# Optimization experiments

Measured on AMD Instinct MI355X. Metric: run time of the kernel, lower is better.

## Reference

```python
import jax, jax.numpy as jnp
import numpy as np

EPSILON = 1e-6
SEARCH_RADIUS = 11 // 2  # search_window_size=11 -> 121 shifts
PATCH_RADIUS = 5 // 2    # patch_size=5 box sum


def shift_stack(t, r):
    # Matches ShiftStack: outer loop x_shift, inner loop y_shift, roll dims (H,W)=(2,3).
    # t: [B,C,H,W] -> [B,C,H,W,(2r+1)^2]
    return jnp.stack(
        [jnp.roll(t, (dy, dx), axis=(2, 3))
         for dx in range(-r, r + 1) for dy in range(-r, r + 1)],
        axis=-1,
    )


def box_sum(t, r):
    # Circular box-filter sum over a (2r+1)x(2r+1) window; separable form is
    # mathematically identical to the original 25 rolls (rolls commute/add).
    s = sum(jnp.roll(t, d, axis=2) for d in range(-r, r + 1))
    return sum(jnp.roll(s, d, axis=3) for d in range(-r, r + 1))


def setup_inputs() -> dict:
    key = jax.random.key(0)
    k1, k2 = jax.random.split(key)
    rgb = jax.random.uniform(k1, (1, 3, 512, 512), dtype=jnp.float32)
    # realistic noise std in [0.02, 0.12]
    sigma = jax.random.uniform(k2, (1, 1, 1, 1), dtype=jnp.float32) * 0.1 + 0.02
    return {"rgb": rgb, "sigma": sigma}


def reference(rgb, sigma):
    h = sigma * 2.0                                     # [B,1,1,1]
    y = 0.299 * rgb[:, :1] + 0.587 * rgb[:, 1:2] + 0.114 * rgb[:, 2:]  # [B,1,H,W]
    rgb_stack = shift_stack(rgb, SEARCH_RADIUS)         # [B,3,H,W,K]
    y_stack = shift_stack(y, SEARCH_RADIUS)             # [B,1,H,W,K]
    sq_diff = (y[..., None] - y_stack) ** 2             # [B,1,H,W,K]
    distances = jnp.sqrt(box_sum(sq_diff, PATCH_RADIUS))
    weights = jnp.exp(-distances / (jax.nn.relu(h)[..., None] + EPSILON))  # [B,1,H,W,K]
    denoised = (weights * rgb_stack).sum(axis=-1) / weights.sum(axis=-1)   # [B,3,H,W]
    return jnp.clip(denoised, 0.0, 1.0)
```

## Files before the change

### kernel.cpp

```cpp
#include <hip/hip_runtime.h>
#include <math.h>

#define IH 512
#define IW 512
#define NPX (IH*IW)

#define TW 60
#define BH 16
#define NXT 9
#define YROWS 30
#define YCOLS 74
#define YSZ2 (YROWS*YCOLS)
#define RROWS 26
#define RCOLS 74
#define RCH2 (RROWS*RCOLS)

#define TS 32
#define YHALO 7
#define RHALO 5
#define YD (TS + 2*YHALO)
#define RD (TS + 2*RHALO)
#define RSZ (RD*RD)
#define MYSZ (YD*YD)

#define FSQRT(x) __builtin_amdgcn_sqrtf(x)
#if __has_builtin(__builtin_amdgcn_exp2f)
#define FEXP2(x) __builtin_amdgcn_exp2f(x)
#else
#define FEXP2(x) exp2f(x)
#endif

__device__ __forceinline__ float dpp_shl1(float x) {
    return __int_as_float(__builtin_amdgcn_update_dpp(
        0, __float_as_int(x), 0x130, 0xf, 0xf, true));
}

__global__ __launch_bounds__(256)
void nlm_part(const float* __restrict__ rgb,
              const float* __restrict__ sigma,
              float4* __restrict__ ws) {
    __shared__ float  YL[YSZ2];
    __shared__ float4 RGBL4[RCH2];

    const int tid   = threadIdx.x;
    const int lane  = tid & 63;
    const int wavei = tid >> 6;
    const int tx0 = blockIdx.x * TW;
    const int ty0 = blockIdx.y * BH;
    const int slice = blockIdx.z;
    const int nz = gridDim.z;

    const float* Rp = rgb;
    const float* Gp = rgb + NPX;
    const float* Bp = rgb + 2*NPX;

    for (int idx = tid; idx < YSZ2; idx += 256) {
        int a = idx / YCOLS, b = idx - a*YCOLS;
        int gy = (ty0 + a - 7) & (IH-1);
        int gx = (tx0 + b - 7) & (IW-1);
        int g = gy*IW + gx;
        YL[idx] = 0.299f*Rp[g] + 0.587f*Gp[g] + 0.114f*Bp[g];
    }
    for (int idx = tid; idx < RCH2; idx += 256) {
        int a = idx / RCOLS, b = idx - a*RCOLS;
        int gy = (ty0 + a - 5) & (IH-1);
        int gx = (tx0 + b - 5) & (IW-1);
        int g = gy*IW + gx;
        RGBL4[idx] = make_float4(Rp[g], Gp[g], Bp[g], 0.f);
    }
    __syncthreads();

    const float m2 = -1.4426950408889634f /
                     (fmaxf(sigma[0]*2.0f, 0.0f) + 1e-6f);

    const int l  = lane;
    const int r0 = wavei*4;

    float yb8[8];
    #pragma unroll
    for (int i = 0; i < 8; ++i)
        yb8[i] = YL[(r0+5+i)*YCOLS + (l+5)];

    float accR[4]={0,0,0,0}, accG[4]={0,0,0,0},
          accB[4]={0,0,0,0}, den[4]={0,0,0,0};

    int dxlo, dxcnt;
    if (nz == 6) { if (slice < 5) { dxlo = -5 + 2*slice; dxcnt = 2; }
                   else           { dxlo = 5;            dxcnt = 1; } }
    else         { if (slice < 3) { dxlo = -5 + 3*slice; dxcnt = 3; }
                   else           { dxlo = 4;            dxcnt = 2; } }

    for (int u = 0; u < dxcnt; ++u) {
        const int dx = dxlo + u;
        const int ysb   = r0*YCOLS + (l + 5 - dx);
        const int rgb_b = r0*RCOLS + (l + 5 - dx);

        float sub8[8];
        #pragma unroll
        for (int j = 0; j < 8; ++j)
            sub8[j] = YL[ysb + j*YCOLS];

        float4 rgbw[4];
        #pragma unroll
        for (int s = 0; s < 4; ++s)
            rgbw[s] = RGBL4[rgb_b + s*RCOLS];

        #pragma unroll
        for (int k = 0; k <= 10; ++k) {
            if (k > 0) {
                sub8[(k+7)&7] = YL[ysb + (7+k)*YCOLS];
                rgbw[(k+3)&3] = RGBL4[rgb_b + (k+3)*RCOLS];
            }
            float pre[9]; pre[0] = 0.f;
            #pragma unroll
            for (int i = 0; i < 8; ++i) {
                float d = yb8[i] - sub8[(i+k)&7];
                pre[i+1] = fmaf(d, d, pre[i]);
            }
            float V[4];
            #pragma unroll
            for (int rr = 0; rr < 4; ++rr) V[rr] = pre[rr+5] - pre[rr];

            float box[4];
            #pragma unroll
            for (int rr = 0; rr < 4; ++rr) {
                float s1 = dpp_shl1(V[rr]);
                float s2 = dpp_shl1(s1);
                float s3 = dpp_shl1(s2);
                float s4 = dpp_shl1(s3);
                box[rr] = ((V[rr] + s1) + (s2 + s3)) + s4;
            }
            #pragma unroll
            for (int rr = 0; rr < 4; ++rr) {
                float w = FEXP2(FSQRT(fmaxf(box[rr], 0.f)) * m2);
                float4 p = rgbw[(k+rr)&3];
                accR[rr] = fmaf(w, p.x, accR[rr]);
                accG[rr] = fmaf(w, p.y, accG[rr]);
                accB[rr] = fmaf(w, p.z, accB[rr]);
                den[rr] += w;
            }
        }
    }

    if (l < TW && tx0 + l < IW) {
        #pragma unroll
        for (int rr = 0; rr < 4; ++rr) {
            int px = (ty0 + r0 + rr)*IW + tx0 + l;
            ws[(size_t)slice*NPX + px] =
                make_float4(accR[rr], accG[rr], accB[rr], den[rr]);
        }
    }
}

__global__ __launch_bounds__(256)
void nlm_combine(const float4* __restrict__ ws, float* __restrict__ out,
                 int nslice) {
    int px = blockIdx.x * 256 + threadIdx.x;
    float r = 0.f, g = 0.f, b = 0.f, w = 0.f;
    for (int s = 0; s < nslice; ++s) {
        float4 v = ws[(size_t)s * NPX + px];
        r += v.x; g += v.y; b += v.z; w += v.w;
    }
    float iw = 1.0f / w;
    out[px]           = fminf(fmaxf(r * iw, 0.f), 1.f);
    out[NPX + px]     = fminf(fmaxf(g * iw, 0.f), 1.f);
    out[2 * NPX + px] = fminf(fmaxf(b * iw, 0.f), 1.f);
}

__global__ __launch_bounds__(256)
void nlm_mono(const float* __restrict__ rgb,
              const float* __restrict__ sigma,
              float* __restrict__ out) {
    __shared__ float Y[MYSZ];
    __shared__ float RGBL[3 * RSZ];

    const int tid = threadIdx.x;
    const int tx0 = blockIdx.x * TS;
    const int ty0 = blockIdx.y * TS;

    const float* Rp = rgb;
    const float* Gp = rgb + NPX;
    const float* Bp = rgb + 2 * NPX;

    for (int idx = tid; idx < MYSZ; idx += 256) {
        int a = idx / YD, b = idx - a * YD;
        int gy = (ty0 + a - YHALO) & (IH - 1);
        int gx = (tx0 + b - YHALO) & (IW - 1);
        int g = gy * IW + gx;
        Y[idx] = 0.299f * Rp[g] + 0.587f * Gp[g] + 0.114f * Bp[g];
    }
    for (int idx = tid; idx < RSZ; idx += 256) {
        int a = idx / RD, b = idx - a * RD;
        int gy = (ty0 + a - RHALO) & (IH - 1);
        int gx = (tx0 + b - RHALO) & (IW - 1);
        int g = gy * IW + gx;
        RGBL[idx]           = Rp[g];
        RGBL[RSZ + idx]     = Gp[g];
        RGBL[2 * RSZ + idx] = Bp[g];
    }
    __syncthreads();

    const float minv_h = -1.0f / (fmaxf(sigma[0] * 2.0f, 0.0f) + 1e-6f);
    const int tx = tid & 31;
    const int tz = tid >> 5;
    const int r0 = tz * 4;

    const int ybase = (YHALO + r0 - 2) * YD + (YHALO + tx - 2);
    float yb[8][5];
    #pragma unroll
    for (int i = 0; i < 8; ++i)
        #pragma unroll
        for (int b = 0; b < 5; ++b)
            yb[i][b] = Y[ybase + i * YD + b];

    float accR[4] = {0.f,0.f,0.f,0.f}, accG[4] = {0.f,0.f,0.f,0.f};
    float accB[4] = {0.f,0.f,0.f,0.f}, den[4] = {0.f,0.f,0.f,0.f};

    for (int dx = -5; dx <= 5; ++dx) {
        const int ybd = (YHALO + r0 - 7) * YD + (YHALO + tx - 2 - dx);
        const int rbd = (RHALO + r0 - 5) * RD + (RHALO + tx - dx);

        #pragma unroll
        for (int k = 0; k <= 10; ++k) {
            float hs[8];
            #pragma unroll
            for (int i = 0; i < 8; ++i) {
                float s = 0.f;
                #pragma unroll
                for (int b = 0; b < 5; ++b) {
                    float d = yb[i][b] - Y[ybd + (i + k) * YD + b];
                    s = fmaf(d, d, s);
                }
                hs[i] = s;
            }
            float pre[9];
            pre[0] = 0.f;
            #pragma unroll
            for (int i = 0; i < 8; ++i) pre[i + 1] = pre[i] + hs[i];
            #pragma unroll
            for (int rr = 0; rr < 4; ++rr) {
                float box = pre[rr + 5] - pre[rr];
                float w = __expf(FSQRT(box) * minv_h);
                const int s2 = rbd + (rr + k) * RD;
                accR[rr] = fmaf(w, RGBL[s2], accR[rr]);
                accG[rr] = fmaf(w, RGBL[RSZ + s2], accG[rr]);
                accB[rr] = fmaf(w, RGBL[2 * RSZ + s2], accB[rr]);
                den[rr] += w;
            }
        }
    }

    #pragma unroll
    for (int rr = 0; rr < 4; ++rr) {
        int px = (ty0 + r0 + rr) * IW + tx0 + tx;
        float iw = 1.0f / den[rr];
        out[px]           = fminf(fmaxf(accR[rr] * iw, 0.f), 1.f);
        out[NPX + px]     = fminf(fmaxf(accG[rr] * iw, 0.f), 1.f);
        out[2 * NPX + px] = fminf(fmaxf(accB[rr] * iw, 0.f), 1.f);
    }
}

extern "C" void kernel_launch(void* const* d_in, const int* in_sizes, int n_in,
                              void* d_out, int out_size, void* d_ws, size_t ws_size,
                              hipStream_t stream) {
    const float* rgb   = (const float*)d_in[0];
    const float* sigma = (const float*)d_in[1];
    float* out = (float*)d_out;

    const size_t need6 = (size_t)6 * NPX * sizeof(float4);
    const size_t need4 = (size_t)4 * NPX * sizeof(float4);
    int nslice = (ws_size >= need6) ? 6 : (ws_size >= need4 ? 4 : 0);

    if (nslice > 0) {
        float4* ws = (float4*)d_ws;
        dim3 grid(NXT, IH / BH, nslice);
        nlm_part<<<grid, dim3(256), 0, stream>>>(rgb, sigma, ws);
        nlm_combine<<<dim3(NPX / 256), dim3(256), 0, stream>>>(ws, out, nslice);
    } else {
        dim3 grid(IW / TS, IH / TS);
        nlm_mono<<<grid, dim3(256), 0, stream>>>(rgb, sigma, out);
    }
}
```

Measured before the change: 41.90 us.

## Read RGB neighbours straight from global memory instead of staging in LDS

Drops the shared-memory RGB tile and its staging loop, and loads R, G, B values directly from global memory (served by L1/L2) with row offsets precomputed per thread. The loads are software-prefetched two rows ahead, and the Y shared-memory reads are prefetched one row ahead. This cuts LDS footprint and the block's prologue, which may raise occupancy. In exchange it issues three global loads per row step instead of one LDS float4 read, so it relies on cache hits and on enough latency hiding.

```diff
diff --git a/kernel.cpp b/kernel.cpp
--- a/kernel.cpp
+++ b/kernel.cpp
@@ -11,9 +11,6 @@
 #define YROWS 30
 #define YCOLS 74
 #define YSZ2 (YROWS*YCOLS)
-#define RROWS 26
-#define RCOLS 74
-#define RCH2 (RROWS*RCOLS)
 
 #define TS 32
 #define YHALO 7
@@ -39,8 +36,7 @@
 void nlm_part(const float* __restrict__ rgb,
               const float* __restrict__ sigma,
               float4* __restrict__ ws) {
-    __shared__ float  YL[YSZ2];
-    __shared__ float4 RGBL4[RCH2];
+    __shared__ float YL[YSZ2];
 
     const int tid   = threadIdx.x;
     const int lane  = tid & 63;
@@ -61,13 +57,6 @@
         int g = gy*IW + gx;
         YL[idx] = 0.299f*Rp[g] + 0.587f*Gp[g] + 0.114f*Bp[g];
     }
-    for (int idx = tid; idx < RCH2; idx += 256) {
-        int a = idx / RCOLS, b = idx - a*RCOLS;
-        int gy = (ty0 + a - 5) & (IH-1);
-        int gx = (tx0 + b - 5) & (IW-1);
-        int g = gy*IW + gx;
-        RGBL4[idx] = make_float4(Rp[g], Gp[g], Bp[g], 0.f);
-    }
     __syncthreads();
 
     const float m2 = -1.4426950408889634f /
@@ -80,6 +69,11 @@
     #pragma unroll
     for (int i = 0; i < 8; ++i)
         yb8[i] = YL[(r0+5+i)*YCOLS + (l+5)];
+
+    int rb[14];
+    #pragma unroll
+    for (int q = 0; q < 14; ++q)
+        rb[q] = ((ty0 + r0 - 5 + q) & (IH-1)) << 9;
 
     float accR[4]={0,0,0,0}, accG[4]={0,0,0,0},
           accB[4]={0,0,0,0}, den[4]={0,0,0,0};
@@ -92,24 +86,37 @@
 
     for (int u = 0; u < dxcnt; ++u) {
         const int dx = dxlo + u;
-        const int ysb   = r0*YCOLS + (l + 5 - dx);
-        const int rgb_b = r0*RCOLS + (l + 5 - dx);
+        const int ysb  = r0*YCOLS + (l + 5 - dx);
+        const int coli = (tx0 + l - dx) & (IW-1);
 
         float sub8[8];
         #pragma unroll
         for (int j = 0; j < 8; ++j)
             sub8[j] = YL[ysb + j*YCOLS];
-
-        float4 rgbw[4];
-        #pragma unroll
-        for (int s = 0; s < 4; ++s)
-            rgbw[s] = RGBL4[rgb_b + s*RCOLS];
+        float nY = YL[ysb + 8*YCOLS];
+
+        float rw[4], gw[4], bw[4];
+        #pragma unroll
+        for (int s = 0; s < 4; ++s) {
+            int o = rb[s] + coli;
+            rw[s] = Rp[o]; gw[s] = Gp[o]; bw[s] = Bp[o];
+        }
+        int oA = rb[4] + coli;
+        float rA = Rp[oA], gA = Gp[oA], bA = Bp[oA];
+        int oB = rb[5] + coli;
+        float rB = Rp[oB], gB = Gp[oB], bB = Bp[oB];
 
         #pragma unroll
         for (int k = 0; k <= 10; ++k) {
             if (k > 0) {
-                sub8[(k+7)&7] = YL[ysb + (7+k)*YCOLS];
-                rgbw[(k+3)&3] = RGBL4[rgb_b + (k+3)*RCOLS];
+                sub8[(k+7)&7] = nY;
+                if (k < 10) nY = YL[ysb + (8+k)*YCOLS];
+                rw[(k+3)&3] = rA; gw[(k+3)&3] = gA; bw[(k+3)&3] = bA;
+                rA = rB; gA = gB; bA = bB;
+                if (k <= 8) {
+                    int o = rb[k+5] + coli;
+                    rB = Rp[o]; gB = Gp[o]; bB = Bp[o];
+                }
             }
             float pre[9]; pre[0] = 0.f;
             #pragma unroll
@@ -133,10 +140,9 @@
             #pragma unroll
             for (int rr = 0; rr < 4; ++rr) {
                 float w = FEXP2(FSQRT(fmaxf(box[rr], 0.f)) * m2);
-                float4 p = rgbw[(k+rr)&3];
-                accR[rr] = fmaf(w, p.x, accR[rr]);
-                accG[rr] = fmaf(w, p.y, accG[rr]);
-                accB[rr] = fmaf(w, p.z, accB[rr]);
+                accR[rr] = fmaf(w, rw[(k+rr)&3], accR[rr]);
+                accG[rr] = fmaf(w, gw[(k+rr)&3], accG[rr]);
+                accB[rr] = fmaf(w, bw[(k+rr)&3], accB[rr]);
                 den[rr] += w;
             }
         }
```

After: 39.98 us. -4.6%, faster.
